# Kernel tuning notes

Measured on AMD Instinct MI355X. Metric: run time of the kernel, lower is better.

## Reference

```python
import jax, jax.numpy as jnp
import numpy as np

B, L, D, DC, DH, H, DE, DO, DT = 4, 2048, 256, 256, 32, 8, 1024, 256, 256


def _ln(x, g, b, eps=1e-5):
    m = jnp.mean(x, -1, keepdims=True)
    v = jnp.mean((x - m) ** 2, -1, keepdims=True)
    return (x - m) * jax.lax.rsqrt(v + eps) * g + b


def setup_inputs() -> dict:
    key = jax.random.key(0)
    ks = jax.random.split(key, 16)

    def p(k, shape, s=0.02):
        return jax.random.normal(k, shape, jnp.float32) * s

    return dict(
        x=jax.random.normal(ks[0], (B, L, D), jnp.float32),
        context=jax.random.normal(ks[1], (B, L, DC), jnp.float32),
        t=jax.random.normal(ks[2], (B, DT), jnp.float32),
        pos_enc=jax.random.normal(ks[3], (1, L, D), jnp.float32),
        ln_g=jnp.ones(D), ln_b=jnp.zeros(D),
        Wq=p(ks[4], (D, DH * H)), bq=jnp.zeros(DH * H),
        Wkv1=p(ks[5], (DC, DC)), bkv1=jnp.zeros(DC),
        kvln_g=jnp.ones(DC), kvln_b=jnp.zeros(DC),
        Wkv2=p(ks[6], (DC, (DH + D) * H)), bkv2=jnp.zeros((DH + D) * H),
        Wm=p(ks[7], (D * H, D)), bm=jnp.zeros(D),
        Wt1=p(ks[8], (DT, DT)), bt1=jnp.zeros(DT),
        Wt2=p(ks[9], (DT, D + DE)), bt2=jnp.zeros(D + DE),
        ff1ln_g=jnp.ones(D), ff1ln_b=jnp.zeros(D),
        Wff1=p(ks[10], (D, DE)), bff1=jnp.zeros(DE),
        Wff2=p(ks[11], (DE, DO)), bff2=jnp.zeros(DO),
    )


def reference(x, context, t, pos_enc, ln_g, ln_b, Wq, bq, Wkv1, bkv1,
              kvln_g, kvln_b, Wkv2, bkv2, Wm, bm, Wt1, bt1, Wt2, bt2,
              ff1ln_g, ff1ln_b, Wff1, bff1, Wff2, bff2):
    silu = jax.nn.silu
    # q_proj = Swish -> Linear, applied to ln(x) + pos_enc
    q = silu(_ln(x, ln_g, ln_b) + pos_enc) @ Wq + bq          # [B,L,H*DH]
    q = q.reshape(B, L, H, DH)
    # kv_proj = Linear -> LayerNorm -> Swish -> Linear
    kv = silu(_ln(context @ Wkv1 + bkv1, kvln_g, kvln_b)) @ Wkv2 + bkv2
    k = kv[..., : DH * H].reshape(B, L, H, DH)
    v = kv[..., DH * H:].reshape(B, L, H, D)                   # v head dim = d_in
    scale = DH ** -0.5
    attn = jnp.einsum('bnhc,bmhc->bhnm', q, k) * scale         # [B,H,L,L]
    # mask = 1 - triu(ones): True strictly BELOW the diagonal (anti-causal)
    mask = jnp.tril(jnp.ones((L, L), bool), -1)
    attn = jnp.where(mask, -jnp.inf, attn)
    attn = jax.nn.softmax(attn, axis=-1)
    out = jnp.einsum('bhnm,bmhc->bnhc', attn, v).reshape(B, L, H * D)
    x = x + out @ Wm + bm
    # FiLM time conditioning: [B, d_in+d_expand] -> [B, 1, ...]
    th = silu(t @ Wt1 + bt1) @ Wt2 + bt2
    t_shift = th[:, None, :D]
    t_scale = th[:, None, D:]
    h = silu(_ln(x + t_shift, ff1ln_g, ff1ln_b)) @ Wff1 + bff1
    # ff2 = Swish -> Dropout(eval) -> Linear; shortcut is Identity (d_in == d_out)
    return silu(h * jax.nn.sigmoid(t_scale)) @ Wff2 + bff2 + x
```

## Files before the change

kernel.cpp:

```cpp
#include <hip/hip_runtime.h>
#include <hip/hip_bf16.h>

#define DEVI __device__ __forceinline__
using u16 = unsigned short;
using u32 = unsigned int;

typedef __attribute__((ext_vector_type(4))) float f32x4;
typedef __attribute__((ext_vector_type(8))) __bf16 bf16x8;

constexpr int L_ = 2048;

DEVI u16 f2bf(float f){
  u32 u = __builtin_bit_cast(u32, f);
  u32 r = u + 0x7FFFu + ((u >> 16) & 1u);
  return (u16)(r >> 16);
}
DEVI float sigm(float x){ return 1.f / (1.f + __expf(-x)); }

DEVI f32x4 mfma16(bf16x8 a, bf16x8 b, f32x4 c){
  return __builtin_amdgcn_mfma_f32_16x16x32_bf16(a, b, c, 0, 0, 0);
}

DEVI void gload16(const u16* src, u16* lds){
  __builtin_amdgcn_global_load_lds(
      (const __attribute__((address_space(1))) u32*)src,
      (__attribute__((address_space(3))) u32*)lds, 16, 0, 0);
}
DEVI void gload4(const u16* src, u16* lds){
  __builtin_amdgcn_global_load_lds(
      (const __attribute__((address_space(1))) u32*)src,
      (__attribute__((address_space(3))) u32*)lds, 4, 0, 0);
}

#define WAITV(N) asm volatile("s_waitcnt vmcnt(" #N ")" ::: "memory")

__global__ __launch_bounds__(256)
void wtrans_all(const float* __restrict__ Wq,   u16* __restrict__ wtq,
                const float* __restrict__ Wkv1, u16* __restrict__ wtkv1,
                const float* __restrict__ Wkv2, u16* __restrict__ wtkv2,
                const float* __restrict__ Wm,   u16* __restrict__ wtm,
                const float* __restrict__ Wff1, u16* __restrict__ wtff1,
                const float* __restrict__ Wff2, u16* __restrict__ wtff2,
                const float* __restrict__ tvec, const float* __restrict__ Wt1,
                const float* __restrict__ bt1,  float* __restrict__ ub){
  __shared__ float smem[32 * 33];
  const int id = blockIdx.x;
  if (id >= 1728){
    int b = id - 1728, j = threadIdx.x;
    smem[j] = tvec[b * 256 + j];
    __syncthreads();
    float acc = bt1[j];
    for (int k = 0; k < 256; ++k) acc += smem[k] * Wt1[k * 256 + j];
    ub[b * 256 + j] = acc * sigm(acc);
    return;
  }
  const float* W; u16* WT; int K, N, local, nx;
  if      (id <   64){ W = Wq;   WT = wtq;   K = 256;  N = 256;  local = id;        nx = 8;  }
  else if (id <  128){ W = Wkv1; WT = wtkv1; K = 256;  N = 256;  local = id - 64;   nx = 8;  }
  else if (id <  704){ W = Wkv2; WT = wtkv2; K = 256;  N = 2304; local = id - 128;  nx = 72; }
  else if (id < 1216){ W = Wm;   WT = wtm;   K = 2048; N = 256;  local = id - 704;  nx = 8;  }
  else if (id < 1472){ W = Wff1; WT = wtff1; K = 256;  N = 1024; local = id - 1216; nx = 32; }
  else               { W = Wff2; WT = wtff2; K = 1024; N = 256;  local = id - 1472; nx = 8;  }
  int n0 = (local % nx) * 32, k0 = (local / nx) * 32;
  float (*tile)[33] = (float(*)[33])smem;
  int tx = threadIdx.x & 31, ty = threadIdx.x >> 5;
  #pragma unroll
  for (int i = 0; i < 4; ++i){ int kk = ty + i*8; tile[kk][tx] = W[(long)(k0+kk)*N + n0 + tx]; }
  __syncthreads();
  #pragma unroll
  for (int i = 0; i < 4; ++i){ int nn = ty + i*8; WT[(long)(n0+nn)*K + k0 + tx] = f2bf(tile[tx][nn]); }
}

__global__ __launch_bounds__(256)
void prep2(const float* __restrict__ ctx, u16* __restrict__ ctx_bf,
           const float* __restrict__ x, const float* __restrict__ pos,
           const float* __restrict__ ln_g, const float* __restrict__ ln_b,
           u16* __restrict__ qin_bf,
           const float* __restrict__ ub, const float* __restrict__ Wt2,
           const float* __restrict__ bt2, float* __restrict__ th){
  __shared__ float us[256];
  const int id = blockIdx.x;
  if (id < 2048){
    long i = ((long)id * 256 + threadIdx.x) * 4;
    float4 v = *(const float4*)(ctx + i);
    ushort4 o; o.x = f2bf(v.x); o.y = f2bf(v.y); o.z = f2bf(v.z); o.w = f2bf(v.w);
    *(ushort4*)(ctx_bf + i) = o;
    return;
  }
  if (id >= 4096){
    int local = id - 4096;
    int b = local & 3, jb = local >> 2;
    int j = jb * 256 + threadIdx.x;
    us[threadIdx.x] = ub[b * 256 + threadIdx.x];
    __syncthreads();
    float acc = bt2[j];
    for (int k = 0; k < 256; ++k) acc += us[k] * Wt2[k * 1280 + j];
    th[b * 1280 + j] = acc;
    return;
  }
  const int row  = (id - 2048) * 4 + (threadIdx.x >> 6);
  const int lane = threadIdx.x & 63;
  const long base = (long)row * 256 + lane * 4;
  float4 x4 = *(const float4*)(x + base);
  float v[4] = {x4.x, x4.y, x4.z, x4.w};
  float s = v[0] + v[1] + v[2] + v[3];
  #pragma unroll
  for (int d = 1; d < 64; d <<= 1) s += __shfl_xor(s, d);
  const float mean = s * (1.f / 256.f);
  float q = 0.f;
  #pragma unroll
  for (int i = 0; i < 4; ++i){ float dd = v[i] - mean; q += dd * dd; }
  #pragma unroll
  for (int d = 1; d < 64; d <<= 1) q += __shfl_xor(q, d);
  const float rstd = rsqrtf(q * (1.f / 256.f) + 1e-5f);
  float4 g4 = *(const float4*)(ln_g + lane * 4);
  float4 b4 = *(const float4*)(ln_b + lane * 4);
  float4 pp = *(const float4*)(pos + (long)(row & (L_ - 1)) * 256 + lane * 4);
  float gv[4] = {g4.x, g4.y, g4.z, g4.w}, bb[4] = {b4.x, b4.y, b4.z, b4.w};
  float pe[4] = {pp.x, pp.y, pp.z, pp.w};
  ushort4 o; u16 tmp[4];
  #pragma unroll
  for (int i = 0; i < 4; ++i){
    float y = (v[i] - mean) * rstd * gv[i] + bb[i] + pe[i];
    y = y * sigm(y);
    tmp[i] = f2bf(y);
  }
  o.x = tmp[0]; o.y = tmp[1]; o.z = tmp[2]; o.w = tmp[3];
  *(ushort4*)(qin_bf + base) = o;
}

template<int MODE>
__global__ __launch_bounds__(256)
void ln_silu(const float* __restrict__ in, const float* __restrict__ add,
             const float* __restrict__ g, const float* __restrict__ bvec,
             u16* __restrict__ out){
  const int row  = blockIdx.x * 4 + (threadIdx.x >> 6);
  const int lane = threadIdx.x & 63;
  const long base = (long)row * 256 + lane * 4;
  float4 x4 = *(const float4*)(in + base);
  float v[4] = {x4.x, x4.y, x4.z, x4.w};
  if constexpr (MODE == 2){
    float4 s4 = *(const float4*)(add + (row >> 11) * 1280 + lane * 4);
    v[0] += s4.x; v[1] += s4.y; v[2] += s4.z; v[3] += s4.w;
  }
  float s = v[0] + v[1] + v[2] + v[3];
  #pragma unroll
  for (int d = 1; d < 64; d <<= 1) s += __shfl_xor(s, d);
  const float mean = s * (1.f / 256.f);
  float q = 0.f;
  #pragma unroll
  for (int i = 0; i < 4; ++i){ float dd = v[i] - mean; q += dd * dd; }
  #pragma unroll
  for (int d = 1; d < 64; d <<= 1) q += __shfl_xor(q, d);
  const float rstd = rsqrtf(q * (1.f / 256.f) + 1e-5f);
  float4 g4 = *(const float4*)(g + lane * 4);
  float4 b4 = *(const float4*)(bvec + lane * 4);
  float gv[4] = {g4.x, g4.y, g4.z, g4.w}, bb[4] = {b4.x, b4.y, b4.z, b4.w};
  ushort4 o; u16 tmp[4];
  #pragma unroll
  for (int i = 0; i < 4; ++i){
    float y = (v[i] - mean) * rstd * gv[i] + bb[i];
    y = y * sigm(y);
    tmp[i] = f2bf(y);
  }
  o.x = tmp[0]; o.y = tmp[1]; o.z = tmp[2]; o.w = tmp[3];
  *(ushort4*)(out + base) = o;
}

template<int EPI>
__global__ __launch_bounds__(512, 4)
void gemm2(const u16* __restrict__ A, const u16* __restrict__ BT,
           const float* __restrict__ bias, const float* __restrict__ res,
           const float* __restrict__ thv,
           float* __restrict__ outF, u16* __restrict__ outB, u16* __restrict__ outB2,
           int M, int N, int K){
  __shared__ u16 smem[3 * 4096 + 3 * 8192];
  u16* As = smem;
  u16* Bs = smem + 3 * 4096;
  const int t = threadIdx.x, lane = t & 63;
  const int lr = lane & 15, lg = lane >> 4;
  const int wv = t >> 6;
  const int wrow = (wv >> 2) * 32;
  const int wcol = (wv & 3) * 32;
  const long bm = (long)blockIdx.x * 64, bn = (long)blockIdx.y * 128;

  auto stage = [&](int step, int buf){
    const int kt = step * 64;
    {
      int o = t * 16;
      int row = o >> 7, cb = o & 127;
      int scb = cb ^ ((row & 7) << 4);
      gload16(&A[(bm + row) * K + kt + (scb >> 1)], &As[buf * 4096 + (o >> 1)]);
    }
    #pragma unroll
    for (int i = 0; i < 2; ++i){
      int o = t * 16 + i * 8192;
      int row = o >> 7, cb = o & 127;
      int scb = cb ^ ((row & 7) << 4);
      gload16(&BT[(bn + row) * K + kt + (scb >> 1)], &Bs[buf * 8192 + (o >> 1)]);
    }
  };

  const f32x4 zero = {0.f, 0.f, 0.f, 0.f};
  f32x4 acc[2][2];
  acc[0][0] = zero; acc[0][1] = zero; acc[1][0] = zero; acc[1][1] = zero;

  const int ns = K >> 6;
  stage(0, 0); stage(1, 1);
  int bufc = 0;
  for (int i = 0; i < ns; ++i){
    if (i + 1 < ns) WAITV(3); else WAITV(0);
    __builtin_amdgcn_s_barrier();
    __builtin_amdgcn_sched_barrier(0);
    if (i + 2 < ns){
      int nb = bufc + 2; if (nb >= 3) nb -= 3;
      stage(i + 2, nb);
    }
    __builtin_amdgcn_s_setprio(1);
    #pragma unroll
    for (int ks = 0; ks < 2; ++ks){
      bf16x8 av[2], bv[2];
      const int cb = (ks * 32 + lg * 8) * 2;
      #pragma unroll
      for (int m = 0; m < 2; ++m){
        int row = wrow + m * 16 + lr;
        av[m] = *(const bf16x8*)((const char*)&As[bufc * 4096] + row * 128 + (cb ^ ((row & 7) << 4)));
      }
      #pragma unroll
      for (int n = 0; n < 2; ++n){
        int row = wcol + n * 16 + lr;
        bv[n] = *(const bf16x8*)((const char*)&Bs[bufc * 8192] + row * 128 + (cb ^ ((row & 7) << 4)));
      }
      #pragma unroll
      for (int m = 0; m < 2; ++m)
        #pragma unroll
        for (int n = 0; n < 2; ++n)
          acc[m][n] = mfma16(av[m], bv[n], acc[m][n]);
    }
    __builtin_amdgcn_s_setprio(0);
    bufc = (bufc + 1 == 3) ? 0 : bufc + 1;
  }

  constexpr float QSC = 0.17677669529663687f * 1.4426950408889634f;

  if constexpr (EPI == 3){
    if (blockIdx.y >= 2){
      __syncthreads();
      u16* tile = smem;
      #pragma unroll
      for (int m = 0; m < 2; ++m)
        #pragma unroll
        for (int n = 0; n < 2; ++n){
          int c_l = wcol + n * 16 + lr;
          long col = bn + c_l;
          int rbase = wrow + m * 16 + lg * 4;
          ushort4 pk;
          u16* pp = (u16*)&pk;
          #pragma unroll
          for (int r = 0; r < 4; ++r)
            pp[r] = f2bf(acc[m][n][r] + bias[col]);
          *(ushort4*)&tile[c_l * 72 + rbase] = pk;
        }
      __syncthreads();
      const int b = (int)(bm >> 11), l0 = (int)(bm & 2047);
      const int hdb = (int)bn - 256;
      const int h = hdb >> 8, d0 = hdb & 255;
      const int dd = t >> 2, lh = (t & 3) * 16;
      u16* dst = outB2 + ((long)((b * 8 + h) * 256 + d0 + dd)) * 2048 + l0 + lh;
      *(uint4*)(dst + 0) = *(const uint4*)&tile[dd * 72 + lh + 0];
      *(uint4*)(dst + 8) = *(const uint4*)&tile[dd * 72 + lh + 8];
      return;
    }
    #pragma unroll
    for (int m = 0; m < 2; ++m)
      #pragma unroll
      for (int n = 0; n < 2; ++n)
        #pragma unroll
        for (int r = 0; r < 4; ++r){
          long row = bm + wrow + m * 16 + lg * 4 + r;
          long col = bn + wcol + n * 16 + lr;
          outB[row * 256 + col] = f2bf(acc[m][n][r] + bias[col]);
        }
    return;
  }

  #pragma unroll
  for (int m = 0; m < 2; ++m)
    #pragma unroll
    for (int n = 0; n < 2; ++n)
      #pragma unroll
      for (int r = 0; r < 4; ++r){
        long row = bm + wrow + m * 16 + lg * 4 + r;
        long col = bn + wcol + n * 16 + lr;
        float v = acc[m][n][r] + bias[col];
        if constexpr (EPI == 0){
          outB[row * N + col] = f2bf(v);
        } else if constexpr (EPI == 1){
          outF[row * N + col] = v;
        } else if constexpr (EPI == 2){
          outF[row * N + col] = v + res[row * N + col];
        } else if constexpr (EPI == 4){
          int b = (int)(row >> 11);
          float ts = thv[b * 1280 + 256 + (int)col];
          float z = v * sigm(ts);
          outB[row * N + col] = f2bf(z * sigm(z));
        } else {
          outB[row * N + col] = f2bf(v * QSC);
        }
      }
}

__global__ __launch_bounds__(512, 2)
void attn7(const u16* __restrict__ Q, const u16* __restrict__ Kb,
           const u16* __restrict__ VT, u16* __restrict__ attout){
  const int bh = blockIdx.x, b = bh >> 3, h = bh & 7;
  const int p  = blockIdx.y;
  const int t  = threadIdx.x;
  const int w  = t >> 6, lane = t & 63, lr = lane & 15, lg = lane >> 4;

  __shared__ u16 Vs[3][256 * 64];
  __shared__ u16 Ks[3][64 * 32];
  __shared__ u16 Ps[8][16 * 64];
  u16* myP = &Ps[w][0];

  const f32x4 zero = {0.f, 0.f, 0.f, 0.f};
  const u16* vbase = VT + (long)bh * 256 * 2048;
  const u16* kbase = Kb + (long)(b * L_) * 256 + h * 32;

  auto stage = [&](int m0, int buf){
    #pragma unroll
    for (int i = 0; i < 4; ++i){
      int ob = t * 16 + i * 8192;
      int d = ob >> 7, cb = ob & 127;
      int scb = cb ^ ((d & 7) << 4);
      gload16(vbase + (long)d * 2048 + m0 + (scb >> 1), &Vs[buf][ob >> 1]);
    }
    #pragma unroll
    for (int i = 0; i < 2; ++i){
      int g = t + i * 512;
      int row = g >> 4, sl = g & 15;
      int scol = ((sl & 3) << 1) + ((((sl >> 2) ^ (row & 3))) << 3);
      gload4(kbase + (long)(m0 + row) * 256 + scol, &Ks[buf][g << 1]);
    }
  };

  for (int half = 0; half < 2; ++half){
    const int chunk = half ? (15 - p) : p;
    const int n0 = chunk * 128;
    const int n_lo = n0 + w * 16;
    const int nt = (L_ - n0) >> 6;

    bf16x8 qf = *(const bf16x8*)(Q + ((long)(b * L_ + n_lo + lr)) * 256 + h * 32 + lg * 8);

    f32x4 o[16];
    #pragma unroll
    for (int c2 = 0; c2 < 16; ++c2) o[c2] = zero;
    float mrun = -1e30f, srun = 0.f;

    stage(n0, 0); stage(n0 + 64, 1);

    int bufc = 0;
    for (int tt = 0; tt < nt; ++tt){
      const int m0 = n0 + tt * 64;
      if (tt + 1 < nt) WAITV(6); else WAITV(0);
      __builtin_amdgcn_s_barrier();
      __builtin_amdgcn_sched_barrier(0);
      if (tt + 2 < nt){
        int nb = bufc + 2; if (nb >= 3) nb -= 3;
        stage(m0 + 128, nb);
      }

      if (m0 + 64 > n_lo){
        const bool partial = (m0 < n_lo + 16);

        bf16x8 kf[4];
        #pragma unroll
        for (int c = 0; c < 4; ++c){
          int row = c * 16 + lr;
          kf[c] = *(const bf16x8*)&Ks[bufc][row * 32 + ((lg ^ (row & 3)) << 3)];
        }
        f32x4 sc[4];
        #pragma unroll
        for (int c = 0; c < 4; ++c)
          sc[c] = mfma16(kf[c], qf, zero);

        if (partial){
          #pragma unroll
          for (int c = 0; c < 4; ++c)
            #pragma unroll
            for (int r = 0; r < 4; ++r)
              if ((m0 + c * 16 + lg * 4 + r) < (n_lo + lr)) sc[c][r] = -1e30f;
        }

        float t0 = fmaxf(fmaxf(sc[0][0], sc[0][1]), fmaxf(sc[0][2], sc[0][3]));
        #pragma unroll
        for (int c = 1; c < 4; ++c)
          t0 = fmaxf(t0, fmaxf(fmaxf(sc[c][0], sc[c][1]), fmaxf(sc[c][2], sc[c][3])));
        t0 = fmaxf(t0, __shfl_xor(t0, 16));
        t0 = fmaxf(t0, __shfl_xor(t0, 32));
        const bool needl = (t0 > mrun + 11.5f);
        if (__any(needl)){
          float mn  = fmaxf(mrun, t0);
          float frc = exp2f(mrun - mn);
          mrun = mn; srun *= frc;
          float f0 = __shfl(frc, lg * 4 + 0), f1 = __shfl(frc, lg * 4 + 1);
          float f2 = __shfl(frc, lg * 4 + 2), f3 = __shfl(frc, lg * 4 + 3);
          f32x4 fv = {f0, f1, f2, f3};
          #pragma unroll
          for (int c2 = 0; c2 < 16; ++c2) o[c2] *= fv;
        }

        {
          const int q = lr, sw = (q & 7) << 3;
          float rs = 0.f;
          #pragma unroll
          for (int c = 0; c < 4; ++c){
            float e0 = exp2f(sc[c][0] - mrun);
            float e1 = exp2f(sc[c][1] - mrun);
            float e2 = exp2f(sc[c][2] - mrun);
            float e3 = exp2f(sc[c][3] - mrun);
            if (partial && mrun < -1e29f){ e0 = e1 = e2 = e3 = 0.f; }
            rs += (e0 + e1) + (e2 + e3);
            ushort4 pk;
            pk.x = __builtin_bit_cast(u16, (__bf16)e0);
            pk.y = __builtin_bit_cast(u16, (__bf16)e1);
            pk.z = __builtin_bit_cast(u16, (__bf16)e2);
            pk.w = __builtin_bit_cast(u16, (__bf16)e3);
            *(ushort4*)&myP[q * 64 + ((c * 16 + lg * 4) ^ sw)] = pk;
          }
          rs += __shfl_xor(rs, 16);
          rs += __shfl_xor(rs, 32);
          srun += rs;
        }

        __builtin_amdgcn_s_setprio(1);
        #pragma unroll
        for (int ks = 0; ks < 2; ++ks){
          bf16x8 pa = *(const bf16x8*)&myP[lr * 64 + ((ks * 32 + lg * 8) ^ ((lr & 7) << 3))];
          #pragma unroll
          for (int c2 = 0; c2 < 16; ++c2){
            const int d = c2 * 16 + lr;
            bf16x8 vf = *(const bf16x8*)((const char*)&Vs[bufc][0] + d * 128 +
                                         ((ks * 64 + lg * 16) ^ ((d & 7) << 4)));
            o[c2] = mfma16(pa, vf, o[c2]);
          }
        }
        __builtin_amdgcn_s_setprio(0);
      }
      bufc = (bufc + 1 == 3) ? 0 : bufc + 1;
    }

    {
      float invc = 1.f / srun;
      #pragma unroll
      for (int r = 0; r < 4; ++r){
        float inv = __shfl(invc, lg * 4 + r);
        long row = (long)(b * L_ + n_lo + lg * 4 + r);
        #pragma unroll
        for (int c2 = 0; c2 < 16; ++c2)
          attout[row * 2048 + h * 256 + c2 * 16 + lr] = f2bf(o[c2][r] * inv);
      }
    }
    WAITV(0);
    __syncthreads();
  }
}

extern "C" void kernel_launch(void* const* d_in, const int* in_sizes, int n_in,
                              void* d_out, int out_size, void* d_ws, size_t ws_size,
                              hipStream_t stream){
  (void)in_sizes; (void)n_in; (void)out_size; (void)ws_size;
  const float* x    = (const float*)d_in[0];
  const float* ctx  = (const float*)d_in[1];
  const float* tin  = (const float*)d_in[2];
  const float* pos  = (const float*)d_in[3];
  const float* ln_g = (const float*)d_in[4];
  const float* ln_b = (const float*)d_in[5];
  const float* Wq   = (const float*)d_in[6];
  const float* bq   = (const float*)d_in[7];
  const float* Wkv1 = (const float*)d_in[8];
  const float* bkv1 = (const float*)d_in[9];
  const float* kvg  = (const float*)d_in[10];
  const float* kvb  = (const float*)d_in[11];
  const float* Wkv2 = (const float*)d_in[12];
  const float* bkv2 = (const float*)d_in[13];
  const float* Wm   = (const float*)d_in[14];
  const float* bm   = (const float*)d_in[15];
  const float* Wt1  = (const float*)d_in[16];
  const float* bt1  = (const float*)d_in[17];
  const float* Wt2  = (const float*)d_in[18];
  const float* bt2  = (const float*)d_in[19];
  const float* fg   = (const float*)d_in[20];
  const float* fb   = (const float*)d_in[21];
  const float* Wff1 = (const float*)d_in[22];
  const float* bff1 = (const float*)d_in[23];
  const float* Wff2 = (const float*)d_in[24];
  const float* bff2 = (const float*)d_in[25];

  char* ws = (char*)d_ws;
  u16*   wt_q   = (u16*)  (ws + 0);
  u16*   wt_kv1 = (u16*)  (ws + 131072);
  u16*   wt_kv2 = (u16*)  (ws + 262144);
  u16*   wt_m   = (u16*)  (ws + 1441792);
  u16*   wt_ff1 = (u16*)  (ws + 2490368);
  u16*   wt_ff2 = (u16*)  (ws + 3014656);
  u16*   ctx_bf = (u16*)  (ws + 3538944);
  u16*   qin_bf = (u16*)  (ws + 7733248);
  u16*   q_bf   = (u16*)  (ws + 11927552);
  float* kv1    = (float*)(ws + 16121856);
  u16*   k_bf   = (u16*)  (ws + 24510464);
  u16*   v_bf   = (u16*)  (ws + 28704768);
  u16*   vT     = (u16*)  (ws + 62259200);
  float* ub     = (float*)(ws + 95813632);
  float* th     = (float*)(ws + 95817728);

  wtrans_all<<<1732, 256, 0, stream>>>(Wq, wt_q, Wkv1, wt_kv1, Wkv2, wt_kv2,
                                       Wm, wt_m, Wff1, wt_ff1, Wff2, wt_ff2,
                                       tin, Wt1, bt1, ub);
  prep2<<<4116, 256, 0, stream>>>(ctx, ctx_bf, x, pos, ln_g, ln_b, qin_bf,
                                  ub, Wt2, bt2, th);
  gemm2<5><<<dim3(128, 2), 512, 0, stream>>>(qin_bf, wt_q, bq, nullptr, nullptr,
                                             nullptr, q_bf, nullptr, 8192, 256, 256);
  gemm2<1><<<dim3(128, 2), 512, 0, stream>>>(ctx_bf, wt_kv1, bkv1, nullptr, nullptr,
                                             kv1, nullptr, nullptr, 8192, 256, 256);
  ln_silu<1><<<2048, 256, 0, stream>>>(kv1, nullptr, kvg, kvb, qin_bf);
  gemm2<3><<<dim3(128, 18), 512, 0, stream>>>(qin_bf, wt_kv2, bkv2, nullptr, nullptr,
                                              nullptr, k_bf, vT, 8192, 2304, 256);
  attn7<<<dim3(32, 8), 512, 0, stream>>>(q_bf, k_bf, vT, v_bf);
  gemm2<2><<<dim3(128, 2), 512, 0, stream>>>(v_bf, wt_m, bm, x, nullptr,
                                             kv1, nullptr, nullptr, 8192, 256, 2048);
  ln_silu<2><<<2048, 256, 0, stream>>>(kv1, th, fg, fb, ctx_bf);
  gemm2<4><<<dim3(128, 8), 512, 0, stream>>>(ctx_bf, wt_ff1, bff1, nullptr, th,
                                             nullptr, (u16*)vT, nullptr, 8192, 1024, 256);
  gemm2<2><<<dim3(128, 2), 512, 0, stream>>>((u16*)vT, wt_ff2, bff2, kv1, nullptr,
                                             (float*)d_out, nullptr, nullptr, 8192, 256, 1024);
}
```

Measured before the change: 192.1 us.

## Split attention warps into query-pairs sharing V halves to reuse V fragments

Each warp now processes 32 query rows and half of the V head dimension instead of 16 rows over the full 256-wide dimension. Each V fragment read from LDS feeds two MFMAs, halving LDS V-read traffic per matrix op in the PV product. In exchange, the QK^T scores, masking and softmax exponentials are computed redundantly by both warps of a pair, and the per-warp P staging buffer doubles in LDS.

```diff
diff --git a/kernel.cpp b/kernel.cpp
--- a/kernel.cpp
+++ b/kernel.cpp
@@ -311,16 +311,18 @@
 }
 
 __global__ __launch_bounds__(512, 2)
-void attn7(const u16* __restrict__ Q, const u16* __restrict__ Kb,
-           const u16* __restrict__ VT, u16* __restrict__ attout){
+void attn10(const u16* __restrict__ Q, const u16* __restrict__ Kb,
+            const u16* __restrict__ VT, u16* __restrict__ attout){
   const int bh = blockIdx.x, b = bh >> 3, h = bh & 7;
   const int p  = blockIdx.y;
   const int t  = threadIdx.x;
   const int w  = t >> 6, lane = t & 63, lr = lane & 15, lg = lane >> 4;
+  const int pr = w >> 1;
+  const int d_base = (w & 1) * 128;
 
   __shared__ u16 Vs[3][256 * 64];
   __shared__ u16 Ks[3][64 * 32];
-  __shared__ u16 Ps[8][16 * 64];
+  __shared__ u16 Ps[8][32 * 64];
   u16* myP = &Ps[w][0];
 
   const f32x4 zero = {0.f, 0.f, 0.f, 0.f};
@@ -347,15 +349,20 @@
   for (int half = 0; half < 2; ++half){
     const int chunk = half ? (15 - p) : p;
     const int n0 = chunk * 128;
-    const int n_lo = n0 + w * 16;
+    const int n_lo = n0 + pr * 32;
     const int nt = (L_ - n0) >> 6;
 
-    bf16x8 qf = *(const bf16x8*)(Q + ((long)(b * L_ + n_lo + lr)) * 256 + h * 32 + lg * 8);
-
-    f32x4 o[16];
-    #pragma unroll
-    for (int c2 = 0; c2 < 16; ++c2) o[c2] = zero;
-    float mrun = -1e30f, srun = 0.f;
+    bf16x8 qf[2];
+    #pragma unroll
+    for (int qh = 0; qh < 2; ++qh)
+      qf[qh] = *(const bf16x8*)(Q + ((long)(b * L_ + n_lo + qh * 16 + lr)) * 256 + h * 32 + lg * 8);
+
+    f32x4 o[2][8];
+    #pragma unroll
+    for (int qh = 0; qh < 2; ++qh)
+      #pragma unroll
+      for (int c2 = 0; c2 < 8; ++c2) o[qh][c2] = zero;
+    float mrun[2] = {-1e30f, -1e30f}, srun[2] = {0.f, 0.f};
 
     stage(n0, 0); stage(n0 + 64, 1);
 
@@ -371,7 +378,7 @@
       }
 
       if (m0 + 64 > n_lo){
-        const bool partial = (m0 < n_lo + 16);
+        const bool partial = (m0 < n_lo + 32);
 
         bf16x8 kf[4];
         #pragma unroll
@@ -379,47 +386,62 @@
           int row = c * 16 + lr;
           kf[c] = *(const bf16x8*)&Ks[bufc][row * 32 + ((lg ^ (row & 3)) << 3)];
         }
-        f32x4 sc[4];
-        #pragma unroll
-        for (int c = 0; c < 4; ++c)
-          sc[c] = mfma16(kf[c], qf, zero);
+        f32x4 sc[2][4];
+        #pragma unroll
+        for (int qh = 0; qh < 2; ++qh)
+          #pragma unroll
+          for (int c = 0; c < 4; ++c)
+            sc[qh][c] = mfma16(kf[c], qf[qh], zero);
 
         if (partial){
           #pragma unroll
-          for (int c = 0; c < 4; ++c)
+          for (int qh = 0; qh < 2; ++qh)
             #pragma unroll
-            for (int r = 0; r < 4; ++r)
-              if ((m0 + c * 16 + lg * 4 + r) < (n_lo + lr)) sc[c][r] = -1e30f;
-        }
-
-        float t0 = fmaxf(fmaxf(sc[0][0], sc[0][1]), fmaxf(sc[0][2], sc[0][3]));
-        #pragma unroll
-        for (int c = 1; c < 4; ++c)
-          t0 = fmaxf(t0, fmaxf(fmaxf(sc[c][0], sc[c][1]), fmaxf(sc[c][2], sc[c][3])));
-        t0 = fmaxf(t0, __shfl_xor(t0, 16));
-        t0 = fmaxf(t0, __shfl_xor(t0, 32));
-        const bool needl = (t0 > mrun + 11.5f);
+            for (int c = 0; c < 4; ++c)
+              #pragma unroll
+              for (int r = 0; r < 4; ++r)
+                if ((m0 + c * 16 + lg * 4 + r) < (n_lo + qh * 16 + lr)) sc[qh][c][r] = -1e30f;
+        }
+
+        float tmax[2]; bool needl = false;
+        #pragma unroll
+        for (int qh = 0; qh < 2; ++qh){
+          float t0 = fmaxf(fmaxf(sc[qh][0][0], sc[qh][0][1]), fmaxf(sc[qh][0][2], sc[qh][0][3]));
+          #pragma unroll
+          for (int c = 1; c < 4; ++c)
+            t0 = fmaxf(t0, fmaxf(fmaxf(sc[qh][c][0], sc[qh][c][1]),
+                                 fmaxf(sc[qh][c][2], sc[qh][c][3])));
+          t0 = fmaxf(t0, __shfl_xor(t0, 16));
+          t0 = fmaxf(t0, __shfl_xor(t0, 32));
+          tmax[qh] = t0;
+          needl |= (t0 > mrun[qh] + 11.5f);
+        }
         if (__any(needl)){
-          float mn  = fmaxf(mrun, t0);
-          float frc = exp2f(mrun - mn);
-          mrun = mn; srun *= frc;
-          float f0 = __shfl(frc, lg * 4 + 0), f1 = __shfl(frc, lg * 4 + 1);
-          float f2 = __shfl(frc, lg * 4 + 2), f3 = __shfl(frc, lg * 4 + 3);
-          f32x4 fv = {f0, f1, f2, f3};
-          #pragma unroll
-          for (int c2 = 0; c2 < 16; ++c2) o[c2] *= fv;
-        }
-
-        {
-          const int q = lr, sw = (q & 7) << 3;
+          #pragma unroll
+          for (int qh = 0; qh < 2; ++qh){
+            float mn  = fmaxf(mrun[qh], tmax[qh]);
+            float frc = exp2f(mrun[qh] - mn);
+            mrun[qh] = mn; srun[qh] *= frc;
+            float f0 = __shfl(frc, lg * 4 + 0), f1 = __shfl(frc, lg * 4 + 1);
+            float f2 = __shfl(frc, lg * 4 + 2), f3 = __shfl(frc, lg * 4 + 3);
+            f32x4 fv = {f0, f1, f2, f3};
+            #pragma unroll
+            for (int c2 = 0; c2 < 8; ++c2) o[qh][c2] *= fv;
+          }
+        }
+
+        #pragma unroll
+        for (int qh = 0; qh < 2; ++qh){
+          const int q = qh * 16 + lr;
+          const int sw = (q & 7) << 3;
           float rs = 0.f;
           #pragma unroll
           for (int c = 0; c < 4; ++c){
-            float e0 = exp2f(sc[c][0] - mrun);
-            float e1 = exp2f(sc[c][1] - mrun);
-            float e2 = exp2f(sc[c][2] - mrun);
-            float e3 = exp2f(sc[c][3] - mrun);
-            if (partial && mrun < -1e29f){ e0 = e1 = e2 = e3 = 0.f; }
+            float e0 = exp2f(sc[qh][c][0] - mrun[qh]);
+            float e1 = exp2f(sc[qh][c][1] - mrun[qh]);
+            float e2 = exp2f(sc[qh][c][2] - mrun[qh]);
+            float e3 = exp2f(sc[qh][c][3] - mrun[qh]);
+            if (partial && mrun[qh] < -1e29f){ e0 = e1 = e2 = e3 = 0.f; }
             rs += (e0 + e1) + (e2 + e3);
             ushort4 pk;
             pk.x = __builtin_bit_cast(u16, (__bf16)e0);
@@ -430,19 +452,26 @@
           }
           rs += __shfl_xor(rs, 16);
           rs += __shfl_xor(rs, 32);
-          srun += rs;
+          srun[qh] += rs;
         }
 
         __builtin_amdgcn_s_setprio(1);
         #pragma unroll
         for (int ks = 0; ks < 2; ++ks){
-          bf16x8 pa = *(const bf16x8*)&myP[lr * 64 + ((ks * 32 + lg * 8) ^ ((lr & 7) << 3))];
-          #pragma unroll
-          for (int c2 = 0; c2 < 16; ++c2){
-            const int d = c2 * 16 + lr;
+          bf16x8 pa[2];
+          #pragma unroll
+          for (int qh = 0; qh < 2; ++qh){
+            const int q = qh * 16 + lr;
+            pa[qh] = *(const bf16x8*)&myP[q * 64 + ((ks * 32 + lg * 8) ^ ((q & 7) << 3))];
+          }
+          #pragma unroll
+          for (int c2 = 0; c2 < 8; ++c2){
+            const int d = d_base + c2 * 16 + lr;
             bf16x8 vf = *(const bf16x8*)((const char*)&Vs[bufc][0] + d * 128 +
                                          ((ks * 64 + lg * 16) ^ ((d & 7) << 4)));
-            o[c2] = mfma16(pa, vf, o[c2]);
+            #pragma unroll
+            for (int qh = 0; qh < 2; ++qh)
+              o[qh][c2] = mfma16(pa[qh], vf, o[qh][c2]);
           }
         }
         __builtin_amdgcn_s_setprio(0);
@@ -450,15 +479,16 @@
       bufc = (bufc + 1 == 3) ? 0 : bufc + 1;
     }
 
-    {
-      float invc = 1.f / srun;
+    #pragma unroll
+    for (int qh = 0; qh < 2; ++qh){
+      float invc = 1.f / srun[qh];
       #pragma unroll
       for (int r = 0; r < 4; ++r){
         float inv = __shfl(invc, lg * 4 + r);
-        long row = (long)(b * L_ + n_lo + lg * 4 + r);
-        #pragma unroll
-        for (int c2 = 0; c2 < 16; ++c2)
-          attout[row * 2048 + h * 256 + c2 * 16 + lr] = f2bf(o[c2][r] * inv);
+        long row = (long)(b * L_ + n_lo + qh * 16 + lg * 4 + r);
+        #pragma unroll
+        for (int c2 = 0; c2 < 8; ++c2)
+          attout[row * 2048 + h * 256 + d_base + c2 * 16 + lr] = f2bf(o[qh][c2][r] * inv);
       }
     }
     WAITV(0);
@@ -526,7 +556,7 @@
   ln_silu<1><<<2048, 256, 0, stream>>>(kv1, nullptr, kvg, kvb, qin_bf);
   gemm2<3><<<dim3(128, 18), 512, 0, stream>>>(qin_bf, wt_kv2, bkv2, nullptr, nullptr,
                                               nullptr, k_bf, vT, 8192, 2304, 256);
-  attn7<<<dim3(32, 8), 512, 0, stream>>>(q_bf, k_bf, vT, v_bf);
+  attn10<<<dim3(32, 8), 512, 0, stream>>>(q_bf, k_bf, vT, v_bf);
   gemm2<2><<<dim3(128, 2), 512, 0, stream>>>(v_bf, wt_m, bm, x, nullptr,
                                              kv1, nullptr, nullptr, 8192, 256, 2048);
   ln_silu<2><<<2048, 256, 0, stream>>>(kv1, th, fg, fb, ctx_bf);
```

Result: slower. 210.2 us (+9.4%).

## Merge Q and KV1 GEMMs into one launch; use smaller-tile GEMM for N=256

Applied to the files above, without the earlier changes.

The q-projection and kv1 GEMMs, which are independent and share a shape, now run in one launch: the first two grid rows compute one and the next two compute the other. This removes a kernel launch and fills the GPU with a larger grid. A new gemm3 kernel with 32-row tiles and 256 threads replaces gemm2 for the two N=256 residual GEMMs, which have long K. It doubles the number of blocks to improve occupancy and load spread, at the cost of reloading B tiles more often per output.

```diff
diff --git a/kernel.cpp b/kernel.cpp
--- a/kernel.cpp
+++ b/kernel.cpp
@@ -168,13 +168,11 @@
 }
 
 template<int EPI>
-__global__ __launch_bounds__(512, 4)
-void gemm2(const u16* __restrict__ A, const u16* __restrict__ BT,
-           const float* __restrict__ bias, const float* __restrict__ res,
-           const float* __restrict__ thv,
-           float* __restrict__ outF, u16* __restrict__ outB, u16* __restrict__ outB2,
-           int M, int N, int K){
-  __shared__ u16 smem[3 * 4096 + 3 * 8192];
+DEVI void gemm_body(const u16* __restrict__ A, const u16* __restrict__ BT,
+                    const float* __restrict__ bias, const float* __restrict__ res,
+                    const float* __restrict__ thv,
+                    float* __restrict__ outF, u16* __restrict__ outB, u16* __restrict__ outB2,
+                    int N, int K, u16* smem, int by){
   u16* As = smem;
   u16* Bs = smem + 3 * 4096;
   const int t = threadIdx.x, lane = t & 63;
@@ -182,7 +180,7 @@
   const int wv = t >> 6;
   const int wrow = (wv >> 2) * 32;
   const int wcol = (wv & 3) * 32;
-  const long bm = (long)blockIdx.x * 64, bn = (long)blockIdx.y * 128;
+  const long bm = (long)blockIdx.x * 64, bn = (long)by * 128;
 
   auto stage = [&](int step, int buf){
     const int kt = step * 64;
@@ -244,7 +242,7 @@
   constexpr float QSC = 0.17677669529663687f * 1.4426950408889634f;
 
   if constexpr (EPI == 3){
-    if (blockIdx.y >= 2){
+    if (by >= 2){
       __syncthreads();
       u16* tile = smem;
       #pragma unroll
@@ -307,6 +305,113 @@
         } else {
           outB[row * N + col] = f2bf(v * QSC);
         }
+      }
+}
+
+template<int EPI>
+__global__ __launch_bounds__(512, 4)
+void gemm2(const u16* __restrict__ A, const u16* __restrict__ BT,
+           const float* __restrict__ bias, const float* __restrict__ res,
+           const float* __restrict__ thv,
+           float* __restrict__ outF, u16* __restrict__ outB, u16* __restrict__ outB2,
+           int M, int N, int K){
+  __shared__ u16 smem[3 * 4096 + 3 * 8192];
+  gemm_body<EPI>(A, BT, bias, res, thv, outF, outB, outB2, N, K, smem, blockIdx.y);
+}
+
+template<int E0, int E1>
+__global__ __launch_bounds__(512, 4)
+void gemm2_dual(const u16* __restrict__ A0, const u16* __restrict__ B0,
+                const float* __restrict__ bias0, u16* __restrict__ out0,
+                const u16* __restrict__ A1, const u16* __restrict__ B1,
+                const float* __restrict__ bias1, float* __restrict__ out1,
+                int N, int K){
+  __shared__ u16 smem[3 * 4096 + 3 * 8192];
+  if (blockIdx.y < 2)
+    gemm_body<E0>(A0, B0, bias0, nullptr, nullptr, nullptr, out0, nullptr, N, K, smem, blockIdx.y);
+  else
+    gemm_body<E1>(A1, B1, bias1, nullptr, nullptr, out1, nullptr, nullptr, N, K, smem, blockIdx.y - 2);
+}
+
+__global__ __launch_bounds__(256, 2)
+void gemm3(const u16* __restrict__ A, const u16* __restrict__ BT,
+           const float* __restrict__ bias, const float* __restrict__ res,
+           float* __restrict__ outF, int M, int N, int K){
+  __shared__ u16 smem[3 * 2048 + 3 * 8192];
+  u16* As = smem;
+  u16* Bs = smem + 3 * 2048;
+  const int t = threadIdx.x, lane = t & 63;
+  const int lr = lane & 15, lg = lane >> 4;
+  const int wcol = (t >> 6) * 32;
+  const long bm = (long)blockIdx.x * 32, bn = (long)blockIdx.y * 128;
+
+  auto stage = [&](int step, int buf){
+    const int kt = step * 64;
+    {
+      int o = t * 16;
+      int row = o >> 7, cb = o & 127;
+      int scb = cb ^ ((row & 7) << 4);
+      gload16(&A[(bm + row) * K + kt + (scb >> 1)], &As[buf * 2048 + (o >> 1)]);
+    }
+    #pragma unroll
+    for (int i = 0; i < 4; ++i){
+      int o = t * 16 + i * 4096;
+      int row = o >> 7, cb = o & 127;
+      int scb = cb ^ ((row & 7) << 4);
+      gload16(&BT[(bn + row) * K + kt + (scb >> 1)], &Bs[buf * 8192 + (o >> 1)]);
+    }
+  };
+
+  const f32x4 zero = {0.f, 0.f, 0.f, 0.f};
+  f32x4 acc[2][2];
+  acc[0][0] = zero; acc[0][1] = zero; acc[1][0] = zero; acc[1][1] = zero;
+
+  const int ns = K >> 6;
+  stage(0, 0); stage(1, 1);
+  int bufc = 0;
+  for (int i = 0; i < ns; ++i){
+    if (i + 1 < ns) WAITV(5); else WAITV(0);
+    __builtin_amdgcn_s_barrier();
+    __builtin_amdgcn_sched_barrier(0);
+    if (i + 2 < ns){
+      int nb = bufc + 2; if (nb >= 3) nb -= 3;
+      stage(i + 2, nb);
+    }
+    __builtin_amdgcn_s_setprio(1);
+    #pragma unroll
+    for (int ks = 0; ks < 2; ++ks){
+      bf16x8 av[2], bv[2];
+      const int cb = (ks * 32 + lg * 8) * 2;
+      #pragma unroll
+      for (int m = 0; m < 2; ++m){
+        int row = m * 16 + lr;
+        av[m] = *(const bf16x8*)((const char*)&As[bufc * 2048] + row * 128 + (cb ^ ((row & 7) << 4)));
+      }
+      #pragma unroll
+      for (int n = 0; n < 2; ++n){
+        int row = wcol + n * 16 + lr;
+        bv[n] = *(const bf16x8*)((const char*)&Bs[bufc * 8192] + row * 128 + (cb ^ ((row & 7) << 4)));
+      }
+      #pragma unroll
+      for (int m = 0; m < 2; ++m)
+        #pragma unroll
+        for (int n = 0; n < 2; ++n)
+          acc[m][n] = mfma16(av[m], bv[n], acc[m][n]);
+    }
+    __builtin_amdgcn_s_setprio(0);
+    bufc = (bufc + 1 == 3) ? 0 : bufc + 1;
+  }
+
+  #pragma unroll
+  for (int m = 0; m < 2; ++m)
+    #pragma unroll
+    for (int n = 0; n < 2; ++n)
+      #pragma unroll
+      for (int r = 0; r < 4; ++r){
+        long row = bm + m * 16 + lg * 4 + r;
+        long col = bn + wcol + n * 16 + lr;
+        float v = acc[m][n][r] + bias[col];
+        outF[row * N + col] = v + res[row * N + col];
       }
 }
 
@@ -519,19 +624,17 @@
                                        tin, Wt1, bt1, ub);
   prep2<<<4116, 256, 0, stream>>>(ctx, ctx_bf, x, pos, ln_g, ln_b, qin_bf,
                                   ub, Wt2, bt2, th);
-  gemm2<5><<<dim3(128, 2), 512, 0, stream>>>(qin_bf, wt_q, bq, nullptr, nullptr,
-                                             nullptr, q_bf, nullptr, 8192, 256, 256);
-  gemm2<1><<<dim3(128, 2), 512, 0, stream>>>(ctx_bf, wt_kv1, bkv1, nullptr, nullptr,
-                                             kv1, nullptr, nullptr, 8192, 256, 256);
+  gemm2_dual<5,1><<<dim3(128, 4), 512, 0, stream>>>(qin_bf, wt_q, bq, q_bf,
+                                                    ctx_bf, wt_kv1, bkv1, kv1,
+                                                    256, 256);
   ln_silu<1><<<2048, 256, 0, stream>>>(kv1, nullptr, kvg, kvb, qin_bf);
   gemm2<3><<<dim3(128, 18), 512, 0, stream>>>(qin_bf, wt_kv2, bkv2, nullptr, nullptr,
                                               nullptr, k_bf, vT, 8192, 2304, 256);
   attn7<<<dim3(32, 8), 512, 0, stream>>>(q_bf, k_bf, vT, v_bf);
-  gemm2<2><<<dim3(128, 2), 512, 0, stream>>>(v_bf, wt_m, bm, x, nullptr,
-                                             kv1, nullptr, nullptr, 8192, 256, 2048);
+  gemm3<<<dim3(256, 2), 256, 0, stream>>>(v_bf, wt_m, bm, x, kv1, 8192, 256, 2048);
   ln_silu<2><<<2048, 256, 0, stream>>>(kv1, th, fg, fb, ctx_bf);
   gemm2<4><<<dim3(128, 8), 512, 0, stream>>>(ctx_bf, wt_ff1, bff1, nullptr, th,
                                              nullptr, (u16*)vT, nullptr, 8192, 1024, 256);
-  gemm2<2><<<dim3(128, 2), 512, 0, stream>>>((u16*)vT, wt_ff2, bff2, kv1, nullptr,
-                                             (float*)d_out, nullptr, nullptr, 8192, 256, 1024);
-}
+  gemm3<<<dim3(256, 2), 256, 0, stream>>>((u16*)vT, wt_ff2, bff2, kv1,
+                                          (float*)d_out, 8192, 256, 1024);
+}
```

Measured after the change: 188.2 us. 2.0% less time.
